# Optimization experiments

Measured on AMD Instinct MI355X. Metric: run time of the kernel, lower is better.

The kernel has to match this reference:

```python
import jax, jax.numpy as jnp
import numpy as np

B, T, E, H = 16, 512, 4096, 8
HD = E // H  # 512; repo requires T <= HD due to mask buffer shape


def setup_inputs() -> dict:
    key = jax.random.key(0)
    ks = jax.random.split(key, 6)
    s_in = 1.0 / np.sqrt(E)
    data = jax.random.normal(ks[0], (B, T, E), dtype=jnp.float32)
    # per-head projection weights stacked: [H, E, HD], no bias (matches nn.Linear(bias=False))
    Wq = jax.random.normal(ks[1], (H, E, HD), dtype=jnp.float32) * s_in
    Wk = jax.random.normal(ks[2], (H, E, HD), dtype=jnp.float32) * s_in
    Wv = jax.random.normal(ks[3], (H, E, HD), dtype=jnp.float32) * s_in
    # output projection Linear(E, E): stored as [in, out] for y @ Wo + bo
    Wo = jax.random.normal(ks[4], (E, E), dtype=jnp.float32) * s_in
    bo = jax.random.normal(ks[5], (E,), dtype=jnp.float32) * 0.01
    return {"data": data, "Wq": Wq, "Wk": Wk, "Wv": Wv, "Wo": Wo, "bo": bo}


def reference(data, Wq, Wk, Wv, Wo, bo):
    # per-head projections: [B,H,T,HD]
    q = jnp.einsum('bte,hed->bhtd', data, Wq)
    k = jnp.einsum('bte,hed->bhtd', data, Wk)
    v = jnp.einsum('bte,hed->bhtd', data, Wv)
    # NOTE: repo scales by sqrt(EMBEDDING_SIZE), not sqrt(head_size)
    scores = jnp.einsum('bhtd,bhsd->bhts', q, k) / jnp.float32(np.sqrt(E))
    causal = jnp.tril(jnp.ones((T, T), dtype=bool))
    scores = jnp.where(causal, scores, jnp.float32(-jnp.inf))
    attn = jax.nn.softmax(scores, axis=-1)  # dropout is identity (p=0 / eval)
    out = jnp.einsum('bhts,bhsd->bhtd', attn, v)
    # concat heads along feature dim: [B,T,H*HD] == [B,T,E]
    out = out.transpose(0, 2, 1, 3).reshape(B, T, E)
    return out @ Wo + bo
```

## Files before the change

### kernel.cpp

```cpp
#include <hip/hip_runtime.h>
#include <stdint.h>

typedef __bf16  bf16x8 __attribute__((ext_vector_type(8)));
typedef unsigned short u16x8 __attribute__((ext_vector_type(8)));
typedef float   f32x4  __attribute__((ext_vector_type(4)));

__device__ __forceinline__ unsigned short f2b(float f) {
  union { float f; uint32_t u; } v; v.f = f;
  uint32_t r = v.u + 0x7fffu + ((v.u >> 16) & 1u);
  return (unsigned short)(r >> 16);
}
__device__ __forceinline__ float b2f(unsigned short u) {
  union { uint32_t u; float f; } v; v.u = ((uint32_t)u) << 16;
  return v.f;
}

#define GLDS16(gp, lp) __builtin_amdgcn_global_load_lds( \
    (const __attribute__((address_space(1))) void*)(gp), \
    (__attribute__((address_space(3))) void*)(lp), 16, 0, 0)

template <class Epi>
__device__ __forceinline__ void gemm256(
    unsigned short* lds,
    const unsigned short* __restrict__ A, int lda,
    const unsigned short* __restrict__ Bt, int ldb,
    int K, int r0, int c0, Epi epi)
{
  const int tid  = threadIdx.x;
  const int lane = tid & 63;
  const int wave = tid >> 6;
  const int wm   = wave >> 2;
  const int wn   = wave & 3;
  const int quad = lane >> 4;
  const int lm   = lane & 15;
  const int sw   = (quad ^ ((lm >> 1) & 3)) * 8;
  const int NT   = K >> 6;

  size_t gA[2], gB[2];
  int ldso[2];
#pragma unroll
  for (int s = 0; s < 2; s++) {
    int ci = wave * 128 + s * 64 + lane;
    int r  = ci >> 2;
    int c  = (ci & 3) ^ ((r >> 1) & 3);
    gA[s]   = (size_t)(r0 + r) * lda + c * 8;
    gB[s]   = (size_t)(c0 + r) * ldb + c * 8;
    ldso[s] = (wave * 2 + s) * 512;
  }

#define STG_A(t, kh) do { if ((t) < NT) {                         \
    int _b = ((t) & 1) * 32768 + (kh) * 8192;                     \
    size_t _ko = (size_t)(t) * 64 + (kh) * 32;                    \
    GLDS16(A + gA[0] + _ko, lds + _b + ldso[0]);                  \
    GLDS16(A + gA[1] + _ko, lds + _b + ldso[1]); } } while (0)
#define STG_B(t, kh) do { if ((t) < NT) {                         \
    int _b = ((t) & 1) * 32768 + 16384 + (kh) * 8192;             \
    size_t _ko = (size_t)(t) * 64 + (kh) * 32;                    \
    GLDS16(Bt + gB[0] + _ko, lds + _b + ldso[0]);                 \
    GLDS16(Bt + gB[1] + _ko, lds + _b + ldso[1]); } } while (0)

  f32x4 acc[8][4];
#pragma unroll
  for (int i = 0; i < 8; i++)
#pragma unroll
    for (int j = 0; j < 4; j++)
      acc[i][j] = (f32x4){0.f, 0.f, 0.f, 0.f};

  STG_A(0, 0); STG_B(0, 0); STG_A(0, 1); STG_B(0, 1);
  STG_A(1, 0); STG_B(1, 0); STG_A(1, 1);
  asm volatile("s_waitcnt vmcnt(6)" ::: "memory");
  __builtin_amdgcn_s_barrier();

  const int arow = (wm * 128 + lm) * 32 + sw;
  const int brow = (wn * 64 + lm) * 32 + sw;

  for (int t = 0; t < NT; ++t) {
    const int Ab = (t & 1) * 32768;
    const int Bb = Ab + 16384;
    bf16x8 a[8], b[2];

#pragma unroll
    for (int i = 0; i < 8; i++) a[i] = *(const bf16x8*)&lds[Ab + arow + i * 512];
    b[0] = *(const bf16x8*)&lds[Bb + brow];
    b[1] = *(const bf16x8*)&lds[Bb + brow + 512];
    STG_B(t + 1, 1);
    __builtin_amdgcn_s_barrier();
    asm volatile("s_waitcnt lgkmcnt(0)" ::: "memory");
    __builtin_amdgcn_s_setprio(1);
#pragma unroll
    for (int i = 0; i < 8; i++) {
      acc[i][0] = __builtin_amdgcn_mfma_f32_16x16x32_bf16(a[i], b[0], acc[i][0], 0, 0, 0);
      acc[i][1] = __builtin_amdgcn_mfma_f32_16x16x32_bf16(a[i], b[1], acc[i][1], 0, 0, 0);
    }
    __builtin_amdgcn_s_setprio(0);
    __builtin_amdgcn_s_barrier();

    b[0] = *(const bf16x8*)&lds[Bb + brow + 1024];
    b[1] = *(const bf16x8*)&lds[Bb + brow + 1536];
    STG_A(t + 2, 0);
    __builtin_amdgcn_s_barrier();
    asm volatile("s_waitcnt lgkmcnt(0)" ::: "memory");
    __builtin_amdgcn_s_setprio(1);
#pragma unroll
    for (int i = 0; i < 8; i++) {
      acc[i][2] = __builtin_amdgcn_mfma_f32_16x16x32_bf16(a[i], b[0], acc[i][2], 0, 0, 0);
      acc[i][3] = __builtin_amdgcn_mfma_f32_16x16x32_bf16(a[i], b[1], acc[i][3], 0, 0, 0);
    }
    __builtin_amdgcn_s_setprio(0);
    __builtin_amdgcn_s_barrier();

#pragma unroll
    for (int i = 0; i < 8; i++) a[i] = *(const bf16x8*)&lds[Ab + 8192 + arow + i * 512];
    b[0] = *(const bf16x8*)&lds[Bb + 8192 + brow];
    b[1] = *(const bf16x8*)&lds[Bb + 8192 + brow + 512];
    STG_B(t + 2, 0);
    __builtin_amdgcn_s_barrier();
    asm volatile("s_waitcnt lgkmcnt(0)" ::: "memory");
    __builtin_amdgcn_s_setprio(1);
#pragma unroll
    for (int i = 0; i < 8; i++) {
      acc[i][0] = __builtin_amdgcn_mfma_f32_16x16x32_bf16(a[i], b[0], acc[i][0], 0, 0, 0);
      acc[i][1] = __builtin_amdgcn_mfma_f32_16x16x32_bf16(a[i], b[1], acc[i][1], 0, 0, 0);
    }
    __builtin_amdgcn_s_setprio(0);
    __builtin_amdgcn_s_barrier();

    b[0] = *(const bf16x8*)&lds[Bb + 8192 + brow + 1024];
    b[1] = *(const bf16x8*)&lds[Bb + 8192 + brow + 1536];
    STG_A(t + 2, 1);
    if (t == NT - 2)     asm volatile("s_waitcnt vmcnt(0)" ::: "memory");
    else if (t < NT - 2) asm volatile("s_waitcnt vmcnt(6)" ::: "memory");
    __builtin_amdgcn_s_barrier();
    asm volatile("s_waitcnt lgkmcnt(0)" ::: "memory");
    __builtin_amdgcn_s_setprio(1);
#pragma unroll
    for (int i = 0; i < 8; i++) {
      acc[i][2] = __builtin_amdgcn_mfma_f32_16x16x32_bf16(a[i], b[0], acc[i][2], 0, 0, 0);
      acc[i][3] = __builtin_amdgcn_mfma_f32_16x16x32_bf16(a[i], b[1], acc[i][3], 0, 0, 0);
    }
    __builtin_amdgcn_s_setprio(0);
    __builtin_amdgcn_s_barrier();
  }

#pragma unroll
  for (int i = 0; i < 8; i++)
#pragma unroll
    for (int j = 0; j < 4; j++)
#pragma unroll
      for (int r = 0; r < 4; r++)
        epi(r0 + wm * 128 + i * 16 + quad * 4 + r, c0 + wn * 64 + j * 16 + lm, acc[i][j][r]);
#undef STG_A
#undef STG_B
}

template <class Epi>
__device__ __forceinline__ void gemm_core(
    const unsigned short* __restrict__ A, int lda,
    const unsigned short* __restrict__ Bt, int ldb,
    int K, int r0, int c0, Epi epi)
{
  extern __shared__ unsigned short sds[];
  unsigned short* As = sds;
  unsigned short* Bs = sds + 128 * 64;
  const int tid  = threadIdx.x;
  const int lane = tid & 63;
  const int wave = tid >> 6;
  const int wr   = (wave >> 1) * 64;
  const int wc   = (wave & 1) * 64;
  const int quad = lane >> 4;
  const int lm   = lane & 15;

  int srow[4], scol[4], sbase[4];
#pragma unroll
  for (int s = 0; s < 4; s++) {
    int chunk = (wave * 4 + s) * 64 + lane;
    srow[s]  = chunk >> 3;
    scol[s]  = ((chunk & 7) ^ (srow[s] & 7)) * 8;
    sbase[s] = (wave * 4 + s) * 512;
  }

  f32x4 acc[4][4];
#pragma unroll
  for (int i = 0; i < 4; i++)
#pragma unroll
    for (int j = 0; j < 4; j++)
      acc[i][j] = (f32x4){0.f, 0.f, 0.f, 0.f};

  for (int k0 = 0; k0 < K; k0 += 64) {
    __syncthreads();
#pragma unroll
    for (int s = 0; s < 4; s++) {
      GLDS16(A  + (size_t)(r0 + srow[s]) * lda + k0 + scol[s], As + sbase[s]);
      GLDS16(Bt + (size_t)(c0 + srow[s]) * ldb + k0 + scol[s], Bs + sbase[s]);
    }
    __syncthreads();
#pragma unroll
    for (int kk = 0; kk < 64; kk += 32) {
      bf16x8 a[4], b[4];
      const int p = (((kk >> 3) + quad) ^ (lm & 7)) * 8;
#pragma unroll
      for (int i = 0; i < 4; i++)
        a[i] = *(const bf16x8*)&As[(wr + i * 16 + lm) * 64 + p];
#pragma unroll
      for (int j = 0; j < 4; j++)
        b[j] = *(const bf16x8*)&Bs[(wc + j * 16 + lm) * 64 + p];
#pragma unroll
      for (int i = 0; i < 4; i++)
#pragma unroll
        for (int j = 0; j < 4; j++)
          acc[i][j] = __builtin_amdgcn_mfma_f32_16x16x32_bf16(a[i], b[j], acc[i][j], 0, 0, 0);
    }
  }
#pragma unroll
  for (int i = 0; i < 4; i++)
#pragma unroll
    for (int j = 0; j < 4; j++)
#pragma unroll
      for (int r = 0; r < 4; r++)
        epi(r0 + wr + i * 16 + quad * 4 + r, c0 + wc + j * 16 + lm, acc[i][j][r]);
}

__global__ __launch_bounds__(256) void cvt_bf16_kernel(const float* __restrict__ in,
                                                       unsigned short* __restrict__ out) {
  size_t i = ((size_t)blockIdx.x * 256 + threadIdx.x) * 8;
  f32x4 a = *(const f32x4*)&in[i];
  f32x4 b = *(const f32x4*)&in[i + 4];
  u16x8 r;
  r[0] = f2b(a[0]); r[1] = f2b(a[1]); r[2] = f2b(a[2]); r[3] = f2b(a[3]);
  r[4] = f2b(b[0]); r[5] = f2b(b[1]); r[6] = f2b(b[2]); r[7] = f2b(b[3]);
  *(u16x8*)&out[i] = r;
}

__global__ __launch_bounds__(256) void tconv_kernel(const float* __restrict__ in,
                                                    unsigned short* __restrict__ out,
                                                    int R, int C) {
  __shared__ unsigned short tile[32][33];
  int r0 = blockIdx.y * 32, c0 = blockIdx.x * 32;
  const float* inz = in + (size_t)blockIdx.z * R * C;
  unsigned short* outz = out + (size_t)blockIdx.z * R * C;
  int tr = threadIdx.x >> 5;
  int tc = threadIdx.x & 31;
#pragma unroll
  for (int s = 0; s < 4; s++) {
    int r = tr + s * 8;
    tile[r][tc] = f2b(inz[(size_t)(r0 + r) * C + c0 + tc]);
  }
  __syncthreads();
#pragma unroll
  for (int s = 0; s < 4; s++) {
    int r = tr + s * 8;
    outz[(size_t)(c0 + r) * R + r0 + tc] = tile[tc][r];
  }
}

__global__ __launch_bounds__(512) void proj_kernel(const unsigned short* __restrict__ data,
                                                   const unsigned short* __restrict__ Wt,
                                                   unsigned short* __restrict__ q,
                                                   unsigned short* __restrict__ k,
                                                   unsigned short* __restrict__ vt) {
  __shared__ unsigned short lds[65536];
  int z = blockIdx.y;
  int p = z >> 3, h = z & 7;
  int r0 = blockIdx.z * 256, c0 = blockIdx.x * 256;
  const unsigned short* Bt = Wt + (size_t)z * 512 * 4096;
  if (p == 0) {
    unsigned short* dst = q + (size_t)h * 8192 * 512;
    gemm256(lds, data, 4096, Bt, 4096, 4096, r0, c0,
            [=](int row, int col, float v) { dst[(size_t)row * 512 + col] = f2b(v); });
  } else if (p == 1) {
    unsigned short* dst = k + (size_t)h * 8192 * 512;
    gemm256(lds, data, 4096, Bt, 4096, 4096, r0, c0,
            [=](int row, int col, float v) { dst[(size_t)row * 512 + col] = f2b(v); });
  } else {
    gemm256(lds, data, 4096, Bt, 4096, 4096, r0, c0,
            [=](int row, int col, float v) {
              vt[(((size_t)(h * 16 + (row >> 9)) * 512 + col) << 9) + (row & 511)] = f2b(v);
            });
  }
}

__global__ __launch_bounds__(256) void score_kernel(const unsigned short* __restrict__ q,
                                                    const unsigned short* __restrict__ k,
                                                    unsigned short* __restrict__ S) {
  int z = blockIdx.z;
  int h = z >> 4, b = z & 15;
  int r0 = blockIdx.y * 128, c0 = blockIdx.x * 128;
  if (c0 > r0 + 127) return;
  const unsigned short* A  = q + ((size_t)h * 8192 + b * 512) * 512;
  const unsigned short* Bt = k + ((size_t)h * 8192 + b * 512) * 512;
  unsigned short* Sz = S + (size_t)z * 262144;
  gemm_core(A, 512, Bt, 512, 512, r0, c0,
            [=](int row, int col, float v) { Sz[(size_t)row * 512 + col] = f2b(v * 0.015625f); });
}

__global__ __launch_bounds__(256) void softmax_kernel(unsigned short* __restrict__ S) {
  int row  = blockIdx.x * 4 + (threadIdx.x >> 6);
  int lane = threadIdx.x & 63;
  int t = row & 511;
  unsigned short* pr = S + (size_t)row * 512;
  u16x8 u = *(const u16x8*)&pr[lane * 8];
  float s[8];
  float m = -1e30f;
#pragma unroll
  for (int jj = 0; jj < 8; jj++) {
    int j = lane * 8 + jj;
    s[jj] = (j <= t) ? b2f(u[jj]) : -1e30f;
    m = fmaxf(m, s[jj]);
  }
#pragma unroll
  for (int o = 32; o > 0; o >>= 1) m = fmaxf(m, __shfl_xor(m, o, 64));
  float l = 0.f;
#pragma unroll
  for (int jj = 0; jj < 8; jj++) {
    int j = lane * 8 + jj;
    s[jj] = (j <= t) ? __expf(s[jj] - m) : 0.f;
    l += s[jj];
  }
#pragma unroll
  for (int o = 32; o > 0; o >>= 1) l += __shfl_xor(l, o, 64);
  float inv = 1.f / l;
  u16x8 r;
#pragma unroll
  for (int jj = 0; jj < 8; jj++) r[jj] = f2b(s[jj] * inv);
  *(u16x8*)&pr[lane * 8] = r;
}

__global__ __launch_bounds__(256) void av_kernel(const unsigned short* __restrict__ S,
                                                 const unsigned short* __restrict__ vt,
                                                 unsigned short* __restrict__ ao) {
  int z = blockIdx.z;
  int h = z >> 4, b = z & 15;
  int r0 = blockIdx.y * 128, c0 = blockIdx.x * 128;
  const unsigned short* A  = S + (size_t)z * 262144;
  const unsigned short* Bt = vt + (size_t)z * 262144;
  int K = r0 + 128;
  gemm_core(A, 512, Bt, 512, K, r0, c0,
            [=](int row, int col, float v) {
              ao[((size_t)(b * 512 + row)) * 4096 + h * 512 + col] = f2b(v);
            });
}

__global__ __launch_bounds__(512) void out_kernel(const unsigned short* __restrict__ ao,
                                                  const unsigned short* __restrict__ Wot,
                                                  const float* __restrict__ bo,
                                                  float* __restrict__ out) {
  __shared__ unsigned short lds[65536];
  int r0 = blockIdx.y * 256, c0 = blockIdx.x * 256;
  gemm256(lds, ao, 4096, Wot, 4096, 4096, r0, c0,
          [=](int row, int col, float v) { out[(size_t)row * 4096 + col] = v + bo[col]; });
}

extern "C" void kernel_launch(void* const* d_in, const int* in_sizes, int n_in,
                              void* d_out, int out_size, void* d_ws, size_t ws_size,
                              hipStream_t stream) {
  const float* data = (const float*)d_in[0];
  const float* Wq = (const float*)d_in[1];
  const float* Wk = (const float*)d_in[2];
  const float* Wv = (const float*)d_in[3];
  const float* Wo = (const float*)d_in[4];
  const float* bo = (const float*)d_in[5];
  float* out = (float*)d_out;

  char* w = (char*)d_ws;
  unsigned short* datab = (unsigned short*)(w);
  unsigned short* Wt    = (unsigned short*)(w + 67108864ULL);
  unsigned short* Wot   = (unsigned short*)(w + 167772160ULL);
  unsigned short* qb    = (unsigned short*)(w + 201326592ULL);
  unsigned short* kb    = (unsigned short*)(w + 268435456ULL);
  unsigned short* vtb   = (unsigned short*)(w + 335544320ULL);
  unsigned short* Sb    = Wt;
  unsigned short* aob   = datab;

  const size_t LDS_BYTES = 2 * 128 * 64 * sizeof(unsigned short);

  cvt_bf16_kernel<<<16384, 256, 0, stream>>>(data, datab);
  tconv_kernel<<<dim3(16, 128, 8), 256, 0, stream>>>(Wq, Wt, 4096, 512);
  tconv_kernel<<<dim3(16, 128, 8), 256, 0, stream>>>(Wk, Wt + (size_t)8 * 2097152, 4096, 512);
  tconv_kernel<<<dim3(16, 128, 8), 256, 0, stream>>>(Wv, Wt + (size_t)16 * 2097152, 4096, 512);
  tconv_kernel<<<dim3(128, 128, 1), 256, 0, stream>>>(Wo, Wot, 4096, 4096);

  proj_kernel<<<dim3(2, 24, 32), 512, 0, stream>>>(datab, Wt, qb, kb, vtb);
  score_kernel<<<dim3(4, 4, 128), 256, LDS_BYTES, stream>>>(qb, kb, Sb);
  softmax_kernel<<<16384, 256, 0, stream>>>(Sb);
  av_kernel<<<dim3(4, 4, 128), 256, LDS_BYTES, stream>>>(Sb, vtb, aob);
  out_kernel<<<dim3(16, 32, 1), 512, 0, stream>>>(aob, Wot, bo, out);
}
```

Baseline: 1.468 ms.

## Software-pipeline LDS fragment reads with MFMA using ping-pong register sets

Result: slower. 1.521 ms (+3.6%).

```diff
diff --git a/kernel.cpp b/kernel.cpp
--- a/kernel.cpp
+++ b/kernel.cpp
@@ -18,6 +18,27 @@
 #define GLDS16(gp, lp) __builtin_amdgcn_global_load_lds( \
     (const __attribute__((address_space(1))) void*)(gp), \
     (__attribute__((address_space(3))) void*)(lp), 16, 0, 0)
+
+
+__device__ __forceinline__ void rd4(bf16x8 dst[4], const unsigned short* lds,
+                                    int base, int row, int step0) {
+#pragma unroll
+  for (int i = 0; i < 4; i++)
+    dst[i] = *(const bf16x8*)&lds[base + row + (step0 + i) * 512];
+}
+
+template <int IO>
+__device__ __forceinline__ void mfma16(const bf16x8 a4[4], const bf16x8 b4[4],
+                                       f32x4 acc[8][4]) {
+  __builtin_amdgcn_s_setprio(1);
+#pragma unroll
+  for (int i = 0; i < 4; i++)
+#pragma unroll
+    for (int j = 0; j < 4; j++)
+      acc[IO + i][j] =
+          __builtin_amdgcn_mfma_f32_16x16x32_bf16(a4[i], b4[j], acc[IO + i][j], 0, 0, 0);
+  __builtin_amdgcn_s_setprio(0);
+}
 
 template <class Epi>
 __device__ __forceinline__ void gemm256(
@@ -66,80 +87,53 @@
     for (int j = 0; j < 4; j++)
       acc[i][j] = (f32x4){0.f, 0.f, 0.f, 0.f};
 
-  STG_A(0, 0); STG_B(0, 0); STG_A(0, 1); STG_B(0, 1);
-  STG_A(1, 0); STG_B(1, 0); STG_A(1, 1);
-  asm volatile("s_waitcnt vmcnt(6)" ::: "memory");
-  __builtin_amdgcn_s_barrier();
-
   const int arow = (wm * 128 + lm) * 32 + sw;
   const int brow = (wn * 64 + lm) * 32 + sw;
 
+  bf16x8 aX[4], aY[4], bX[4], bY[4];
+
+  STG_B(0, 0); STG_A(0, 0); STG_B(0, 1); STG_A(0, 1);
+  STG_B(1, 0); STG_A(1, 0); STG_B(1, 1);
+  asm volatile("s_waitcnt vmcnt(10)" ::: "memory");
+  __builtin_amdgcn_s_barrier();
+  __builtin_amdgcn_sched_barrier(0);
+  rd4(aX, lds, 0, arow, 0);
+  rd4(bX, lds, 16384, brow, 0);
+
   for (int t = 0; t < NT; ++t) {
-    const int Ab = (t & 1) * 32768;
-    const int Bb = Ab + 16384;
-    bf16x8 a[8], b[2];
-
-#pragma unroll
-    for (int i = 0; i < 8; i++) a[i] = *(const bf16x8*)&lds[Ab + arow + i * 512];
-    b[0] = *(const bf16x8*)&lds[Bb + brow];
-    b[1] = *(const bf16x8*)&lds[Bb + brow + 512];
-    STG_B(t + 1, 1);
+    const int cb = (t & 1) * 32768;
+    const int nb = cb ^ 32768;
+
     __builtin_amdgcn_s_barrier();
-    asm volatile("s_waitcnt lgkmcnt(0)" ::: "memory");
-    __builtin_amdgcn_s_setprio(1);
-#pragma unroll
-    for (int i = 0; i < 8; i++) {
-      acc[i][0] = __builtin_amdgcn_mfma_f32_16x16x32_bf16(a[i], b[0], acc[i][0], 0, 0, 0);
-      acc[i][1] = __builtin_amdgcn_mfma_f32_16x16x32_bf16(a[i], b[1], acc[i][1], 0, 0, 0);
-    }
-    __builtin_amdgcn_s_setprio(0);
+    __builtin_amdgcn_sched_barrier(0);
+    STG_A(t + 1, 1);
+    rd4(aY, lds, cb, arow, 4);
+    mfma16<0>(aX, bX, acc);
+    if (t < NT - 1) asm volatile("s_waitcnt vmcnt(8)" ::: "memory");
+    else            asm volatile("s_waitcnt vmcnt(0)" ::: "memory");
+
     __builtin_amdgcn_s_barrier();
-
-    b[0] = *(const bf16x8*)&lds[Bb + brow + 1024];
-    b[1] = *(const bf16x8*)&lds[Bb + brow + 1536];
+    __builtin_amdgcn_sched_barrier(0);
+    STG_B(t + 2, 0);
+    rd4(aX, lds, cb + 8192, arow, 0);
+    rd4(bY, lds, cb + 16384 + 8192, brow, 0);
+    mfma16<4>(aY, bX, acc);
+
+    __builtin_amdgcn_s_barrier();
+    __builtin_amdgcn_sched_barrier(0);
     STG_A(t + 2, 0);
+    rd4(aY, lds, cb + 8192, arow, 4);
+    mfma16<0>(aX, bY, acc);
+    if      (t < NT - 2) asm volatile("s_waitcnt vmcnt(8)" ::: "memory");
+    else if (t == NT - 2) asm volatile("s_waitcnt vmcnt(4)" ::: "memory");
+    else                 asm volatile("s_waitcnt vmcnt(0)" ::: "memory");
+
     __builtin_amdgcn_s_barrier();
-    asm volatile("s_waitcnt lgkmcnt(0)" ::: "memory");
-    __builtin_amdgcn_s_setprio(1);
-#pragma unroll
-    for (int i = 0; i < 8; i++) {
-      acc[i][2] = __builtin_amdgcn_mfma_f32_16x16x32_bf16(a[i], b[0], acc[i][2], 0, 0, 0);
-      acc[i][3] = __builtin_amdgcn_mfma_f32_16x16x32_bf16(a[i], b[1], acc[i][3], 0, 0, 0);
-    }
-    __builtin_amdgcn_s_setprio(0);
-    __builtin_amdgcn_s_barrier();
-
-#pragma unroll
-    for (int i = 0; i < 8; i++) a[i] = *(const bf16x8*)&lds[Ab + 8192 + arow + i * 512];
-    b[0] = *(const bf16x8*)&lds[Bb + 8192 + brow];
-    b[1] = *(const bf16x8*)&lds[Bb + 8192 + brow + 512];
-    STG_B(t + 2, 0);
-    __builtin_amdgcn_s_barrier();
-    asm volatile("s_waitcnt lgkmcnt(0)" ::: "memory");
-    __builtin_amdgcn_s_setprio(1);
-#pragma unroll
-    for (int i = 0; i < 8; i++) {
-      acc[i][0] = __builtin_amdgcn_mfma_f32_16x16x32_bf16(a[i], b[0], acc[i][0], 0, 0, 0);
-      acc[i][1] = __builtin_amdgcn_mfma_f32_16x16x32_bf16(a[i], b[1], acc[i][1], 0, 0, 0);
-    }
-    __builtin_amdgcn_s_setprio(0);
-    __builtin_amdgcn_s_barrier();
-
-    b[0] = *(const bf16x8*)&lds[Bb + 8192 + brow + 1024];
-    b[1] = *(const bf16x8*)&lds[Bb + 8192 + brow + 1536];
-    STG_A(t + 2, 1);
-    if (t == NT - 2)     asm volatile("s_waitcnt vmcnt(0)" ::: "memory");
-    else if (t < NT - 2) asm volatile("s_waitcnt vmcnt(6)" ::: "memory");
-    __builtin_amdgcn_s_barrier();
-    asm volatile("s_waitcnt lgkmcnt(0)" ::: "memory");
-    __builtin_amdgcn_s_setprio(1);
-#pragma unroll
-    for (int i = 0; i < 8; i++) {
-      acc[i][2] = __builtin_amdgcn_mfma_f32_16x16x32_bf16(a[i], b[0], acc[i][2], 0, 0, 0);
-      acc[i][3] = __builtin_amdgcn_mfma_f32_16x16x32_bf16(a[i], b[1], acc[i][3], 0, 0, 0);
-    }
-    __builtin_amdgcn_s_setprio(0);
-    __builtin_amdgcn_s_barrier();
+    __builtin_amdgcn_sched_barrier(0);
+    STG_B(t + 2, 1);
+    rd4(aX, lds, nb, arow, 0);
+    rd4(bX, lds, nb + 16384, brow, 0);
+    mfma16<4>(aY, bY, acc);
   }
 
 #pragma unroll
```
